# Kernel tuning notes

Hardware: AMD Instinct MI355X
Metric: run time of the kernel (lower is better)

Reference implementation:

```python
import jax, jax.numpy as jnp
import numpy as np

N_AGENTS, T, B, S = 8, 128, 64, 16
D_STATE, E, HH = 128, 64, 128


def _hyper(x, k1, b1, k2, b2):
    return jax.nn.relu(x @ k1 + b1) @ k2 + b2


def _perm_pos(n_agents, tb, s):
    # pos[row, a] = position of agent a in a random grand-coalition permutation
    keys = jax.random.split(jax.random.key(42), tb * s)
    pos = jax.vmap(lambda k: jax.random.permutation(k, n_agents))(keys)
    return pos.reshape(tb, s, n_agents)


def setup_inputs() -> dict:
    key = jax.random.key(0)
    ks = jax.random.split(key, 12)
    def rn(k, shape, scale=0.05):
        return jax.random.normal(k, shape, jnp.float32) * scale
    return {
        "q_vals": rn(ks[0], (N_AGENTS, T, B), 1.0),
        "states": rn(ks[1], (T * B, D_STATE), 1.0),
        "hw1_k1": rn(ks[2], (D_STATE, HH)), "hw1_b1": jnp.zeros((HH,), jnp.float32),
        "hw1_k2": rn(ks[3], (HH, 2 * E)), "hw1_b2": jnp.zeros((2 * E,), jnp.float32),
        "b1_k": rn(ks[4], (D_STATE, E)), "b1_b": jnp.zeros((E,), jnp.float32),
        "hw2_k1": rn(ks[5], (D_STATE, HH)), "hw2_b1": jnp.zeros((HH,), jnp.float32),
        "hw2_k2": rn(ks[6], (HH, E)), "hw2_b2": jnp.zeros((E,), jnp.float32),
        "hb2_k1": rn(ks[7], (D_STATE, E)), "hb2_b1": jnp.zeros((E,), jnp.float32),
        "hb2_k2": rn(ks[8], (E, 1)), "hb2_b2": jnp.zeros((1,), jnp.float32),
    }


def _forward(pos, q_vals, states, hw1_k1, hw1_b1, hw1_k2, hw1_b2, b1_k, b1_b,
             hw2_k1, hw2_b1, hw2_k2, hw2_b2, hb2_k1, hb2_b1, hb2_k2, hb2_b2):
    n, t, b = q_vals.shape
    tb = t * b
    q = jnp.transpose(q_vals, (1, 2, 0)).reshape(tb, n)          # agent_qs, (tb, n)
    qb = jnp.broadcast_to(q[:, None, :], (tb, S, n))
    inv = jnp.argsort(pos, axis=-1)                               # agent at each position
    q_ord = jnp.take_along_axis(qb, inv, axis=-1)                 # q ordered by position
    csum_excl = jnp.cumsum(q_ord, axis=-1) - q_ord                # sum over strictly-earlier positions
    coal_sum = jnp.take_along_axis(csum_excl, pos, axis=-1)       # sum of preceding agents' q
    coal_norm = coal_sum / jnp.maximum(pos, 1).astype(q.dtype)    # mean (0 if no predecessors)
    # Hypernets depend only on states -> compute once per tb row, broadcast over (S, n)
    w1 = jnp.abs(_hyper(states, hw1_k1, hw1_b1, hw1_k2, hw1_b2)).reshape(tb, 1, 1, 2, E)
    b1 = (states @ b1_k + b1_b).reshape(tb, 1, 1, E)
    w2 = jnp.abs(_hyper(states, hw2_k1, hw2_b1, hw2_k2, hw2_b2)).reshape(tb, 1, 1, E)
    b2 = _hyper(states, hb2_k1, hb2_b1, hb2_k2, hb2_b2).reshape(tb, 1, 1)
    hidden = jax.nn.elu(coal_norm[..., None] * w1[..., 0, :]
                        + qb[..., None] * w1[..., 1, :] + b1)     # (tb, S, n, E)
    y = jnp.sum(hidden * w2, axis=-1) + b2                        # (tb, S, n)
    alpha = jnp.abs(y).reshape(t, b, S, n).mean(axis=2)           # mean over samples
    return jnp.transpose(alpha, (2, 0, 1))                        # (n, t, b)


def reference(q_vals, states, hw1_k1, hw1_b1, hw1_k2, hw1_b2, b1_k, b1_b,
              hw2_k1, hw2_b1, hw2_k2, hw2_b2, hb2_k1, hb2_b1, hb2_k2, hb2_b2):
    n, t, b = q_vals.shape
    pos = _perm_pos(n, t * b, S)
    return _forward(pos, q_vals, states, hw1_k1, hw1_b1, hw1_k2, hw1_b2, b1_k, b1_b,
                    hw2_k1, hw2_b1, hw2_k2, hw2_b2, hb2_k1, hb2_b1, hb2_k2, hb2_b2)
```

## Files before the change

kernel.cpp:

```cpp
#include <hip/hip_runtime.h>
#include <stdint.h>

#define N_AG   8
#define S_SAMP 16
#define TB     8192
#define DST    128
#define E_DIM  64

#define RPB    8
#define CN_STR 9

#define WT1K1  0
#define WT2K1  16384
#define WT1K2  32768
#define WTM3   49152
#define WT2K2  65536
#define WT_ELEMS 73728

typedef __attribute__((ext_vector_type(8))) short  short8v;
typedef __attribute__((ext_vector_type(4))) float  float4v;

__device__ __forceinline__ float4 ld4(const float* p) { return *(const float4*)p; }

__device__ __forceinline__ unsigned short f2bf(float f) {
  uint32_t x = __float_as_uint(f);
  return (unsigned short)((x + 0x7FFFu + ((x >> 16) & 1u)) >> 16);
}
__device__ __forceinline__ uint32_t pk2(float lo, float hi) {
  return (uint32_t)f2bf(lo) | ((uint32_t)f2bf(hi) << 16);
}

__device__ __forceinline__ uint2 tf2x32(uint32_t k0, uint32_t k1,
                                        uint32_t c0, uint32_t c1) {
  uint32_t ks2 = k0 ^ k1 ^ 0x1BD11BDAu;
  uint32_t x0 = c0 + k0, x1 = c1 + k1;
#define TFR(r) { x0 += x1; x1 = (x1 << (r)) | (x1 >> (32 - (r))); x1 ^= x0; }
  TFR(13) TFR(15) TFR(26) TFR(6)
  x0 += k1;  x1 += ks2 + 1u;
  TFR(17) TFR(29) TFR(16) TFR(24)
  x0 += ks2; x1 += k0 + 2u;
  TFR(13) TFR(15) TFR(26) TFR(6)
  x0 += k0;  x1 += k1 + 3u;
  TFR(17) TFR(29) TFR(16) TFR(24)
  x0 += k1;  x1 += ks2 + 4u;
  TFR(13) TFR(15) TFR(26) TFR(6)
  x0 += ks2; x1 += k0 + 5u;
#undef TFR
  return make_uint2(x0, x1);
}

__device__ __forceinline__ short8v rdfrag(const unsigned short* base, int row, int ks, int lhi) {
  const int b = (row * 256 + ks * 64 + lhi * 16) ^ ((row & 7) << 4);
  return *(const short8v*)((const char*)base + b);
}
__device__ __forceinline__ void wrbf(unsigned short* pan, int r, int c, float v) {
  const int b = (r * 256 + c * 2) ^ ((r & 7) << 4);
  *(unsigned short*)((char*)pan + b) = f2bf(v);
}
__device__ __forceinline__ short8v gfrag(const unsigned short* wt, int n, int ks, int lhi) {
  return *(const short8v*)(wt + (n << 7) + ks * 32 + lhi * 8);
}

__global__ __launch_bounds__(256)
void wt_transpose(const float* __restrict__ hw1_k1, const float* __restrict__ hw2_k1,
                  const float* __restrict__ hw1_k2, const float* __restrict__ b1_k,
                  const float* __restrict__ hb2_k1, const float* __restrict__ hw2_k2,
                  unsigned short* __restrict__ wt)
{
  __shared__ float t[32][33];
  const int b = blockIdx.x;
  const float* src; int ldn, t0, dstbase;
  if (b < 16)      { src = hw1_k1; ldn = 128; t0 = b;      dstbase = WT1K1; }
  else if (b < 32) { src = hw2_k1; ldn = 128; t0 = b - 16; dstbase = WT2K1; }
  else if (b < 48) { src = hw1_k2; ldn = 128; t0 = b - 32; dstbase = WT1K2; }
  else if (b < 56) { src = b1_k;   ldn = 64;  t0 = b - 48; dstbase = WTM3; }
  else if (b < 64) { src = hb2_k1; ldn = 64;  t0 = b - 56; dstbase = WTM3 + 64 * 128; }
  else             { src = hw2_k2; ldn = 64;  t0 = b - 64; dstbase = WT2K2; }
  const int kt = t0 & 3, nt = t0 >> 2;
  const int tid = threadIdx.x;
  {
    const int c = tid & 31;
    for (int r = tid >> 5; r < 32; r += 8)
      t[r][c] = src[(size_t)(kt * 32 + r) * ldn + nt * 32 + c];
  }
  __syncthreads();
  {
    const int c2 = tid & 15;
    for (int n = tid >> 4; n < 32; n += 16) {
      const uint32_t v = pk2(t[2 * c2][n], t[2 * c2 + 1][n]);
      *(uint32_t*)&wt[dstbase + (nt * 32 + n) * 128 + kt * 32 + 2 * c2] = v;
    }
  }
}

__global__ __launch_bounds__(256, 4)
void alpha_mfma2(const float* __restrict__ q_vals,
                 const float* __restrict__ states,
                 const float* __restrict__ hw1_b1, const float* __restrict__ hw1_b2,
                 const float* __restrict__ b1_b,   const float* __restrict__ hw2_b1,
                 const float* __restrict__ hw2_b2, const float* __restrict__ hb2_b1,
                 const float* __restrict__ hb2_k2, const float* __restrict__ hb2_b2,
                 const unsigned short* __restrict__ wt,
                 float* __restrict__ out)
{
  __shared__ unsigned short xbf[RPB * 128];
  __shared__ unsigned short h1bf[RPB * 128];
  __shared__ unsigned short h2bf[RPB * 128];
  __shared__ float w1l[RPB][132];
  __shared__ float b1l[RPB][68];
  __shared__ float w2l[RPB][68];
  __shared__ float hbl[RPB][68];
  __shared__ float b2l[RPB];
  __shared__ float ql[RPB][N_AG];
  __shared__ float cn_l[RPB][S_SAMP][CN_STR];

  const int tid  = threadIdx.x;
  const int row0 = blockIdx.x * RPB;
  const int lane = tid & 63;
  const int wv   = tid >> 6;
  const int lrow = lane & 15;
  const int lhi  = lane >> 4;

  {
    const int r = tid >> 5, k0 = (tid & 31) * 4;
    const float4 v = ld4(&states[(size_t)(row0 + r) * DST + k0]);
    const int b = (r * 256 + k0 * 2) ^ ((r & 7) << 4);
    *(uint32_t*)((char*)xbf + b)     = pk2(v.x, v.y);
    *(uint32_t*)((char*)xbf + b + 4) = pk2(v.z, v.w);
  }
  if (tid < RPB * N_AG) {
    const int rr = tid >> 3, a = tid & 7;
    ql[rr][a] = q_vals[a * TB + row0 + rr];
  }
  __syncthreads();

  if (tid < RPB * S_SAMP) {
    const int r  = tid >> 4;
    const int sl = tid & 15;
    const uint32_t j = (uint32_t)(row0 + r) * (uint32_t)S_SAMP + (uint32_t)sl;
    uint2 kj  = tf2x32(0u, 42u, 0u, j);
    uint2 sub = tf2x32(kj.x, kj.y, 0u, 1u);
    uint32_t K[N_AG];
#pragma unroll
    for (int i = 0; i < N_AG; ++i) {
      uint2 b = tf2x32(sub.x, sub.y, 0u, (uint32_t)i);
      K[i] = b.x ^ b.y;
    }
    int posa[N_AG];
#pragma unroll
    for (int i = 0; i < N_AG; ++i) {
      int rank = 0;
#pragma unroll
      for (int m = 0; m < N_AG; ++m)
        rank += (K[m] < K[i]) || (K[m] == K[i] && m < i);
      posa[rank] = i;
    }
#pragma unroll
    for (int a = 0; a < N_AG; ++a) {
      const int pa = posa[a];
      float cs = 0.f;
#pragma unroll
      for (int a2 = 0; a2 < N_AG; ++a2)
        cs += (posa[a2] < pa) ? ql[r][a2] : 0.f;
      cn_l[r][sl][a] = cs / (float)max(pa, 1);
    }
  }

  {
    float4v a0 = {0.f,0.f,0.f,0.f}, a1 = {0.f,0.f,0.f,0.f};
    const int c0 = wv * 32 + lrow, c1 = c0 + 16;
#pragma unroll
    for (int ks = 0; ks < 4; ++ks) {
      const short8v af  = rdfrag(xbf, lrow & 7, ks, lhi);
      const short8v b0  = gfrag(wt + WT1K1, c0, ks, lhi);
      const short8v b1f = gfrag(wt + WT1K1, c1, ks, lhi);
      a0 = __builtin_amdgcn_mfma_f32_16x16x32_bf16(af, b0,  a0, 0, 0, 0);
      a1 = __builtin_amdgcn_mfma_f32_16x16x32_bf16(af, b1f, a1, 0, 0, 0);
    }
    if (lhi < 2) {
      const float bv0 = hw1_b1[c0], bv1 = hw1_b1[c1];
#pragma unroll
      for (int j = 0; j < 4; ++j) {
        const int r = lhi * 4 + j;
        wrbf(h1bf, r, c0, fmaxf(a0[j] + bv0, 0.f));
        wrbf(h1bf, r, c1, fmaxf(a1[j] + bv1, 0.f));
      }
    }
  }

  {
    float4v a0 = {0.f,0.f,0.f,0.f}, a1 = {0.f,0.f,0.f,0.f};
    const int c0 = wv * 32 + lrow, c1 = c0 + 16;
#pragma unroll
    for (int ks = 0; ks < 4; ++ks) {
      const short8v af  = rdfrag(xbf, lrow & 7, ks, lhi);
      const short8v b0  = gfrag(wt + WT2K1, c0, ks, lhi);
      const short8v b1f = gfrag(wt + WT2K1, c1, ks, lhi);
      a0 = __builtin_amdgcn_mfma_f32_16x16x32_bf16(af, b0,  a0, 0, 0, 0);
      a1 = __builtin_amdgcn_mfma_f32_16x16x32_bf16(af, b1f, a1, 0, 0, 0);
    }
    if (lhi < 2) {
      const float bv0 = hw2_b1[c0], bv1 = hw2_b1[c1];
#pragma unroll
      for (int j = 0; j < 4; ++j) {
        const int r = lhi * 4 + j;
        wrbf(h2bf, r, c0, fmaxf(a0[j] + bv0, 0.f));
        wrbf(h2bf, r, c1, fmaxf(a1[j] + bv1, 0.f));
      }
    }
  }

  {
    float4v a0 = {0.f,0.f,0.f,0.f}, a1 = {0.f,0.f,0.f,0.f};
    const int c0 = wv * 32 + lrow, c1 = c0 + 16;
#pragma unroll
    for (int ks = 0; ks < 4; ++ks) {
      const short8v af  = rdfrag(xbf, lrow & 7, ks, lhi);
      const short8v b0  = gfrag(wt + WTM3, c0, ks, lhi);
      const short8v b1f = gfrag(wt + WTM3, c1, ks, lhi);
      a0 = __builtin_amdgcn_mfma_f32_16x16x32_bf16(af, b0,  a0, 0, 0, 0);
      a1 = __builtin_amdgcn_mfma_f32_16x16x32_bf16(af, b1f, a1, 0, 0, 0);
    }
    if (lhi < 2) {
#pragma unroll
      for (int j = 0; j < 4; ++j) {
        const int r = lhi * 4 + j;
        if (c0 < 64) b1l[r][c0] = a0[j] + b1_b[c0];
        else         hbl[r][c0 - 64] = fmaxf(a0[j] + hb2_b1[c0 - 64], 0.f);
        if (c1 < 64) b1l[r][c1] = a1[j] + b1_b[c1];
        else         hbl[r][c1 - 64] = fmaxf(a1[j] + hb2_b1[c1 - 64], 0.f);
      }
    }
  }
  __syncthreads();

  if (tid < RPB * S_SAMP) {
    const int r = tid >> 4, sl = tid & 15;
    float v = hbl[r][sl]      * hb2_k2[sl]
            + hbl[r][sl + 16] * hb2_k2[sl + 16]
            + hbl[r][sl + 32] * hb2_k2[sl + 32]
            + hbl[r][sl + 48] * hb2_k2[sl + 48];
    v += __shfl_down(v, 8, 16); v += __shfl_down(v, 4, 16);
    v += __shfl_down(v, 2, 16); v += __shfl_down(v, 1, 16);
    if (sl == 0) b2l[r] = v + hb2_b2[0];
  }

  {
    float4v a0 = {0.f,0.f,0.f,0.f}, a1 = {0.f,0.f,0.f,0.f};
    const int c0 = wv * 32 + lrow, c1 = c0 + 16;
#pragma unroll
    for (int ks = 0; ks < 4; ++ks) {
      const short8v af  = rdfrag(h1bf, lrow & 7, ks, lhi);
      const short8v b0  = gfrag(wt + WT1K2, c0, ks, lhi);
      const short8v b1f = gfrag(wt + WT1K2, c1, ks, lhi);
      a0 = __builtin_amdgcn_mfma_f32_16x16x32_bf16(af, b0,  a0, 0, 0, 0);
      a1 = __builtin_amdgcn_mfma_f32_16x16x32_bf16(af, b1f, a1, 0, 0, 0);
    }
    if (lhi < 2) {
      const float bv0 = hw1_b2[c0], bv1 = hw1_b2[c1];
#pragma unroll
      for (int j = 0; j < 4; ++j) {
        const int r = lhi * 4 + j;
        w1l[r][c0] = fabsf(a0[j] + bv0);
        w1l[r][c1] = fabsf(a1[j] + bv1);
      }
    }
  }

  {
    float4v a0 = {0.f,0.f,0.f,0.f};
    const int c = wv * 16 + lrow;
#pragma unroll
    for (int ks = 0; ks < 4; ++ks) {
      const short8v af = rdfrag(h2bf, lrow & 7, ks, lhi);
      const short8v b0 = gfrag(wt + WT2K2, c, ks, lhi);
      a0 = __builtin_amdgcn_mfma_f32_16x16x32_bf16(af, b0, a0, 0, 0, 0);
    }
    if (lhi < 2) {
      const float bv = hw2_b2[c];
#pragma unroll
      for (int j = 0; j < 4; ++j)
        w2l[lhi * 4 + j][c] = fabsf(a0[j] + bv);
    }
  }
  __syncthreads();

  {
    const int sl = tid & 15;
    const int r  = (tid >> 4) & 7;
    const int a0i = (tid >> 7) * 4;
    float cn[4], qv[4], y[4];
#pragma unroll
    for (int jj = 0; jj < 4; ++jj) {
      cn[jj] = cn_l[r][sl][a0i + jj];
      qv[jj] = ql[r][a0i + jj];
      y[jj]  = 0.f;
    }
#pragma unroll 4
    for (int e = 0; e < E_DIM; e += 4) {
      const float4 wa  = ld4(&w1l[r][e]);
      const float4 wb  = ld4(&w1l[r][64 + e]);
      const float4 bb  = ld4(&b1l[r][e]);
      const float4 w2v = ld4(&w2l[r][e]);
#pragma unroll
      for (int jj = 0; jj < 4; ++jj) {
        float h;
        h = fmaf(cn[jj], wa.x, fmaf(qv[jj], wb.x, bb.x));
        y[jj] = fmaf((h > 0.f) ? h : (__expf(h) - 1.f), w2v.x, y[jj]);
        h = fmaf(cn[jj], wa.y, fmaf(qv[jj], wb.y, bb.y));
        y[jj] = fmaf((h > 0.f) ? h : (__expf(h) - 1.f), w2v.y, y[jj]);
        h = fmaf(cn[jj], wa.z, fmaf(qv[jj], wb.z, bb.z));
        y[jj] = fmaf((h > 0.f) ? h : (__expf(h) - 1.f), w2v.z, y[jj]);
        h = fmaf(cn[jj], wa.w, fmaf(qv[jj], wb.w, bb.w));
        y[jj] = fmaf((h > 0.f) ? h : (__expf(h) - 1.f), w2v.w, y[jj]);
      }
    }
    const float b2v = b2l[r];
#pragma unroll
    for (int jj = 0; jj < 4; ++jj)
      cn_l[r][sl][a0i + jj] = fabsf(y[jj] + b2v);
  }
  __syncthreads();

  if (tid < RPB * N_AG) {
    const int rr = tid & 7, a = tid >> 3;
    float acc = 0.f;
#pragma unroll
    for (int ss = 0; ss < S_SAMP; ++ss) acc += cn_l[rr][ss][a];
    out[a * TB + row0 + rr] = acc * (1.0f / (float)S_SAMP);
  }
}

#define FB_RPB 16
#define FB_H_PAD 132
#define FB_E_PAD 68
__global__ __launch_bounds__(256)
void alpha_fused2(const float* __restrict__ q_vals, const float* __restrict__ states,
                  const float* __restrict__ hw1_k1, const float* __restrict__ hw1_b1,
                  const float* __restrict__ hw1_k2, const float* __restrict__ hw1_b2,
                  const float* __restrict__ b1_k,   const float* __restrict__ b1_b,
                  const float* __restrict__ hw2_k1, const float* __restrict__ hw2_b1,
                  const float* __restrict__ hw2_k2, const float* __restrict__ hw2_b2,
                  const float* __restrict__ hb2_k1, const float* __restrict__ hb2_b1,
                  const float* __restrict__ hb2_k2, const float* __restrict__ hb2_b2,
                  float* __restrict__ out)
{
  __shared__ float s_lds[FB_RPB][DST];
  __shared__ float scratch[FB_RPB][FB_H_PAD];
  __shared__ float scratch2[FB_RPB][FB_E_PAD];
  __shared__ float w1l[FB_RPB][FB_H_PAD];
  __shared__ float b1l[FB_RPB][FB_E_PAD];
  __shared__ float w2l[FB_RPB][FB_E_PAD];
  __shared__ float b2l[FB_RPB];
  __shared__ float qlf[FB_RPB][N_AG];
  __shared__ float cnred[FB_RPB][S_SAMP][N_AG];
  const int tid = threadIdx.x;
  const int row0 = blockIdx.x * FB_RPB;
  const int r = tid >> 4, sl = tid & 15;
  {
    const float4* src = reinterpret_cast<const float4*>(states + (size_t)row0 * DST);
    reinterpret_cast<float4*>(&s_lds[0][0])[tid]       = src[tid];
    reinterpret_cast<float4*>(&s_lds[0][0])[tid + 256] = src[tid + 256];
  }
  if (tid < FB_RPB * N_AG) {
    const int rr = tid >> 3, a = tid & 7;
    qlf[rr][a] = q_vals[a * TB + row0 + rr];
  }
  __syncthreads();
  {
    const uint32_t j = (uint32_t)(row0 + r) * (uint32_t)S_SAMP + (uint32_t)sl;
    uint2 kj = tf2x32(0u, 42u, 0u, j);
    uint2 sub = tf2x32(kj.x, kj.y, 0u, 1u);
    uint32_t K[N_AG];
#pragma unroll
    for (int i = 0; i < N_AG; ++i) { uint2 b = tf2x32(sub.x, sub.y, 0u, (uint32_t)i); K[i] = b.x ^ b.y; }
    int posa[N_AG];
#pragma unroll
    for (int i = 0; i < N_AG; ++i) {
      int rank = 0;
#pragma unroll
      for (int m = 0; m < N_AG; ++m) rank += (K[m] < K[i]) || (K[m] == K[i] && m < i);
      posa[rank] = i;
    }
#pragma unroll
    for (int a = 0; a < N_AG; ++a) {
      const int pa = posa[a];
      float cs = 0.f;
#pragma unroll
      for (int a2 = 0; a2 < N_AG; ++a2) cs += (posa[a2] < pa) ? qlf[r][a2] : 0.f;
      cnred[r][sl][a] = cs / (float)max(pa, 1);
    }
  }
  {
    int c = tid & 127, rg = tid >> 7;
    float a0=0.f,a1=0.f,a2=0.f,a3=0.f,a4=0.f,a5=0.f,a6=0.f,a7=0.f;
#pragma unroll 2
    for (int k = 0; k < DST; ++k) {
      float wv = hw1_k1[k * 128 + c];
      a0 += s_lds[rg*8+0][k]*wv; a1 += s_lds[rg*8+1][k]*wv;
      a2 += s_lds[rg*8+2][k]*wv; a3 += s_lds[rg*8+3][k]*wv;
      a4 += s_lds[rg*8+4][k]*wv; a5 += s_lds[rg*8+5][k]*wv;
      a6 += s_lds[rg*8+6][k]*wv; a7 += s_lds[rg*8+7][k]*wv;
    }
    float b = hw1_b1[c];
    scratch[rg*8+0][c]=fmaxf(a0+b,0.f); scratch[rg*8+1][c]=fmaxf(a1+b,0.f);
    scratch[rg*8+2][c]=fmaxf(a2+b,0.f); scratch[rg*8+3][c]=fmaxf(a3+b,0.f);
    scratch[rg*8+4][c]=fmaxf(a4+b,0.f); scratch[rg*8+5][c]=fmaxf(a5+b,0.f);
    scratch[rg*8+6][c]=fmaxf(a6+b,0.f); scratch[rg*8+7][c]=fmaxf(a7+b,0.f);
  }
  {
    int c = tid & 63, rg = tid >> 6;
    float a0=0.f,a1=0.f,a2=0.f,a3=0.f;
#pragma unroll 2
    for (int k = 0; k < DST; ++k) {
      float wv = b1_k[k * 64 + c];
      a0 += s_lds[rg*4+0][k]*wv; a1 += s_lds[rg*4+1][k]*wv;
      a2 += s_lds[rg*4+2][k]*wv; a3 += s_lds[rg*4+3][k]*wv;
    }
    float b = b1_b[c];
    b1l[rg*4+0][c]=a0+b; b1l[rg*4+1][c]=a1+b; b1l[rg*4+2][c]=a2+b; b1l[rg*4+3][c]=a3+b;
  }
  __syncthreads();
  {
    int c = tid & 127, rg = tid >> 7;
    float a0=0.f,a1=0.f,a2=0.f,a3=0.f,a4=0.f,a5=0.f,a6=0.f,a7=0.f;
#pragma unroll 2
    for (int k = 0; k < DST; ++k) {
      float wv = hw1_k2[k * 128 + c];
      a0 += scratch[rg*8+0][k]*wv; a1 += scratch[rg*8+1][k]*wv;
      a2 += scratch[rg*8+2][k]*wv; a3 += scratch[rg*8+3][k]*wv;
      a4 += scratch[rg*8+4][k]*wv; a5 += scratch[rg*8+5][k]*wv;
      a6 += scratch[rg*8+6][k]*wv; a7 += scratch[rg*8+7][k]*wv;
    }
    float b = hw1_b2[c];
    w1l[rg*8+0][c]=fabsf(a0+b); w1l[rg*8+1][c]=fabsf(a1+b);
    w1l[rg*8+2][c]=fabsf(a2+b); w1l[rg*8+3][c]=fabsf(a3+b);
    w1l[rg*8+4][c]=fabsf(a4+b); w1l[rg*8+5][c]=fabsf(a5+b);
    w1l[rg*8+6][c]=fabsf(a6+b); w1l[rg*8+7][c]=fabsf(a7+b);
  }
  {
    int c = tid & 63, rg = tid >> 6;
    float a0=0.f,a1=0.f,a2=0.f,a3=0.f;
#pragma unroll 2
    for (int k = 0; k < DST; ++k) {
      float wv = hb2_k1[k * 64 + c];
      a0 += s_lds[rg*4+0][k]*wv; a1 += s_lds[rg*4+1][k]*wv;
      a2 += s_lds[rg*4+2][k]*wv; a3 += s_lds[rg*4+3][k]*wv;
    }
    float b = hb2_b1[c];
    scratch2[rg*4+0][c]=fmaxf(a0+b,0.f); scratch2[rg*4+1][c]=fmaxf(a1+b,0.f);
    scratch2[rg*4+2][c]=fmaxf(a2+b,0.f); scratch2[rg*4+3][c]=fmaxf(a3+b,0.f);
  }
  __syncthreads();
  {
    int c = tid & 127, rg = tid >> 7;
    float a0=0.f,a1=0.f,a2=0.f,a3=0.f,a4=0.f,a5=0.f,a6=0.f,a7=0.f;
#pragma unroll 2
    for (int k = 0; k < DST; ++k) {
      float wv = hw2_k1[k * 128 + c];
      a0 += s_lds[rg*8+0][k]*wv; a1 += s_lds[rg*8+1][k]*wv;
      a2 += s_lds[rg*8+2][k]*wv; a3 += s_lds[rg*8+3][k]*wv;
      a4 += s_lds[rg*8+4][k]*wv; a5 += s_lds[rg*8+5][k]*wv;
      a6 += s_lds[rg*8+6][k]*wv; a7 += s_lds[rg*8+7][k]*wv;
    }
    float b = hw2_b1[c];
    scratch[rg*8+0][c]=fmaxf(a0+b,0.f); scratch[rg*8+1][c]=fmaxf(a1+b,0.f);
    scratch[rg*8+2][c]=fmaxf(a2+b,0.f); scratch[rg*8+3][c]=fmaxf(a3+b,0.f);
    scratch[rg*8+4][c]=fmaxf(a4+b,0.f); scratch[rg*8+5][c]=fmaxf(a5+b,0.f);
    scratch[rg*8+6][c]=fmaxf(a6+b,0.f); scratch[rg*8+7][c]=fmaxf(a7+b,0.f);
  }
  if (tid < FB_RPB * S_SAMP) {
    float v = scratch2[r][sl]      * hb2_k2[sl]
            + scratch2[r][sl + 16] * hb2_k2[sl + 16]
            + scratch2[r][sl + 32] * hb2_k2[sl + 32]
            + scratch2[r][sl + 48] * hb2_k2[sl + 48];
    v += __shfl_down(v, 8, 16); v += __shfl_down(v, 4, 16);
    v += __shfl_down(v, 2, 16); v += __shfl_down(v, 1, 16);
    if (sl == 0) b2l[r] = v + hb2_b2[0];
  }
  __syncthreads();
  {
    int c = tid & 63, rg = tid >> 6;
    float a0=0.f,a1=0.f,a2=0.f,a3=0.f;
#pragma unroll 2
    for (int k = 0; k < DST; ++k) {
      float wv = hw2_k2[k * 64 + c];
      a0 += scratch[rg*4+0][k]*wv; a1 += scratch[rg*4+1][k]*wv;
      a2 += scratch[rg*4+2][k]*wv; a3 += scratch[rg*4+3][k]*wv;
    }
    float b = hw2_b2[c];
    w2l[rg*4+0][c]=fabsf(a0+b); w2l[rg*4+1][c]=fabsf(a1+b);
    w2l[rg*4+2][c]=fabsf(a2+b); w2l[rg*4+3][c]=fabsf(a3+b);
  }
  __syncthreads();
  {
    float cn[N_AG], qv[N_AG], y[N_AG];
#pragma unroll
    for (int a = 0; a < N_AG; ++a) { cn[a]=cnred[r][sl][a]; qv[a]=qlf[r][a]; y[a]=0.f; }
#pragma unroll 4
    for (int e = 0; e < E_DIM; e += 4) {
      const float4 wa  = ld4(&w1l[r][e]);
      const float4 wb  = ld4(&w1l[r][64 + e]);
      const float4 bb  = ld4(&b1l[r][e]);
      const float4 w2v = ld4(&w2l[r][e]);
#pragma unroll
      for (int a = 0; a < N_AG; ++a) {
        float h;
        h = fmaf(cn[a], wa.x, fmaf(qv[a], wb.x, bb.x));
        y[a] = fmaf((h > 0.f) ? h : (__expf(h) - 1.f), w2v.x, y[a]);
        h = fmaf(cn[a], wa.y, fmaf(qv[a], wb.y, bb.y));
        y[a] = fmaf((h > 0.f) ? h : (__expf(h) - 1.f), w2v.y, y[a]);
        h = fmaf(cn[a], wa.z, fmaf(qv[a], wb.z, bb.z));
        y[a] = fmaf((h > 0.f) ? h : (__expf(h) - 1.f), w2v.z, y[a]);
        h = fmaf(cn[a], wa.w, fmaf(qv[a], wb.w, bb.w));
        y[a] = fmaf((h > 0.f) ? h : (__expf(h) - 1.f), w2v.w, y[a]);
      }
    }
    const float b2v = b2l[r];
#pragma unroll
    for (int a = 0; a < N_AG; ++a) cnred[r][sl][a] = fabsf(y[a] + b2v);
  }
  __syncthreads();
  if (tid < FB_RPB * N_AG) {
    const int a = tid >> 4, rr = tid & 15;
    float acc = 0.f;
#pragma unroll
    for (int ss = 0; ss < S_SAMP; ++ss) acc += cnred[rr][ss][a];
    out[a * TB + row0 + rr] = acc * (1.0f / (float)S_SAMP);
  }
}

extern "C" void kernel_launch(void* const* d_in, const int* in_sizes, int n_in,
                              void* d_out, int out_size, void* d_ws, size_t ws_size,
                              hipStream_t stream) {
  const float* q_vals = (const float*)d_in[0];
  const float* states = (const float*)d_in[1];
  const float* hw1_k1 = (const float*)d_in[2];
  const float* hw1_b1 = (const float*)d_in[3];
  const float* hw1_k2 = (const float*)d_in[4];
  const float* hw1_b2 = (const float*)d_in[5];
  const float* b1_k   = (const float*)d_in[6];
  const float* b1_b   = (const float*)d_in[7];
  const float* hw2_k1 = (const float*)d_in[8];
  const float* hw2_b1 = (const float*)d_in[9];
  const float* hw2_k2 = (const float*)d_in[10];
  const float* hw2_b2 = (const float*)d_in[11];
  const float* hb2_k1 = (const float*)d_in[12];
  const float* hb2_b1 = (const float*)d_in[13];
  const float* hb2_k2 = (const float*)d_in[14];
  const float* hb2_b2 = (const float*)d_in[15];
  float* out = (float*)d_out;

  const size_t need = (size_t)WT_ELEMS * sizeof(unsigned short);
  if (ws_size >= need) {
    unsigned short* wt = (unsigned short*)d_ws;
    wt_transpose<<<dim3(72), 256, 0, stream>>>(
        hw1_k1, hw2_k1, hw1_k2, b1_k, hb2_k1, hw2_k2, wt);
    alpha_mfma2<<<dim3(TB / RPB), 256, 0, stream>>>(
        q_vals, states, hw1_b1, hw1_b2, b1_b, hw2_b1, hw2_b2, hb2_b1,
        hb2_k2, hb2_b2, wt, out);
  } else {
    alpha_fused2<<<dim3(TB / FB_RPB), 256, 0, stream>>>(
        q_vals, states, hw1_k1, hw1_b1, hw1_k2, hw1_b2, b1_k, b1_b,
        hw2_k1, hw2_b1, hw2_k2, hw2_b2, hb2_k1, hb2_b1, hb2_k2, hb2_b2, out);
  }
}
```

Baseline: 41.64 us.

## Process 16 rows per block with 512 threads to fill MFMA row tiles

Doubles rows per block from 8 to 16 and threads from 256 to 512, so each 16x16 MFMA tile uses all 16 A-rows instead of wasting half on duplicated rows. Each wave now computes a single 16-column output tile per GEMM, and the later elementwise and reduction stages are remapped to the new row and thread counts. Per-row weight fragment loads from global memory are amortised over twice as many rows. The cost is a larger shared-memory footprint and fewer, bigger blocks (512 blocks), which may reduce occupancy. The parts of the kernel not shown (state staging, permutation code) must also handle 16 rows, which cannot be confirmed here.

```diff
diff --git a/kernel.cpp b/kernel.cpp
--- a/kernel.cpp
+++ b/kernel.cpp
@@ -7,7 +7,7 @@
 #define DST    128
 #define E_DIM  64
 
-#define RPB    8
+#define RPB    16
 #define CN_STR 9
 
 #define WT1K1  0
@@ -93,8 +93,8 @@
   }
 }
 
-__global__ __launch_bounds__(256, 4)
-void alpha_mfma2(const float* __restrict__ q_vals,
+__global__ __launch_bounds__(512, 4)
+void alpha_mfma3(const float* __restrict__ q_vals,
                  const float* __restrict__ states,
                  const float* __restrict__ hw1_b1, const float* __restrict__ hw1_b2,
                  const float* __restrict__ b1_b,   const float* __restrict__ hw2_b1,
@@ -167,69 +167,51 @@
   }
 
   {
-    float4v a0 = {0.f,0.f,0.f,0.f}, a1 = {0.f,0.f,0.f,0.f};
-    const int c0 = wv * 32 + lrow, c1 = c0 + 16;
+    float4v a0 = {0.f,0.f,0.f,0.f};
+    const int c = wv * 16 + lrow;
 #pragma unroll
     for (int ks = 0; ks < 4; ++ks) {
-      const short8v af  = rdfrag(xbf, lrow & 7, ks, lhi);
-      const short8v b0  = gfrag(wt + WT1K1, c0, ks, lhi);
-      const short8v b1f = gfrag(wt + WT1K1, c1, ks, lhi);
-      a0 = __builtin_amdgcn_mfma_f32_16x16x32_bf16(af, b0,  a0, 0, 0, 0);
-      a1 = __builtin_amdgcn_mfma_f32_16x16x32_bf16(af, b1f, a1, 0, 0, 0);
-    }
-    if (lhi < 2) {
-      const float bv0 = hw1_b1[c0], bv1 = hw1_b1[c1];
-#pragma unroll
-      for (int j = 0; j < 4; ++j) {
-        const int r = lhi * 4 + j;
-        wrbf(h1bf, r, c0, fmaxf(a0[j] + bv0, 0.f));
-        wrbf(h1bf, r, c1, fmaxf(a1[j] + bv1, 0.f));
-      }
-    }
-  }
-
-  {
-    float4v a0 = {0.f,0.f,0.f,0.f}, a1 = {0.f,0.f,0.f,0.f};
-    const int c0 = wv * 32 + lrow, c1 = c0 + 16;
+      const short8v af = rdfrag(xbf, lrow, ks, lhi);
+      a0 = __builtin_amdgcn_mfma_f32_16x16x32_bf16(af, gfrag(wt + WT1K1, c, ks, lhi), a0, 0, 0, 0);
+    }
+    const float bv = hw1_b1[c];
+#pragma unroll
+    for (int j = 0; j < 4; ++j)
+      wrbf(h1bf, lhi * 4 + j, c, fmaxf(a0[j] + bv, 0.f));
+  }
+
+  {
+    float4v a0 = {0.f,0.f,0.f,0.f};
+    const int c = wv * 16 + lrow;
 #pragma unroll
     for (int ks = 0; ks < 4; ++ks) {
-      const short8v af  = rdfrag(xbf, lrow & 7, ks, lhi);
-      const short8v b0  = gfrag(wt + WT2K1, c0, ks, lhi);
-      const short8v b1f = gfrag(wt + WT2K1, c1, ks, lhi);
-      a0 = __builtin_amdgcn_mfma_f32_16x16x32_bf16(af, b0,  a0, 0, 0, 0);
-      a1 = __builtin_amdgcn_mfma_f32_16x16x32_bf16(af, b1f, a1, 0, 0, 0);
-    }
-    if (lhi < 2) {
-      const float bv0 = hw2_b1[c0], bv1 = hw2_b1[c1];
-#pragma unroll
-      for (int j = 0; j < 4; ++j) {
-        const int r = lhi * 4 + j;
-        wrbf(h2bf, r, c0, fmaxf(a0[j] + bv0, 0.f));
-        wrbf(h2bf, r, c1, fmaxf(a1[j] + bv1, 0.f));
-      }
-    }
-  }
-
-  {
-    float4v a0 = {0.f,0.f,0.f,0.f}, a1 = {0.f,0.f,0.f,0.f};
-    const int c0 = wv * 32 + lrow, c1 = c0 + 16;
+      const short8v af = rdfrag(xbf, lrow, ks, lhi);
+      a0 = __builtin_amdgcn_mfma_f32_16x16x32_bf16(af, gfrag(wt + WT2K1, c, ks, lhi), a0, 0, 0, 0);
+    }
+    const float bv = hw2_b1[c];
+#pragma unroll
+    for (int j = 0; j < 4; ++j)
+      wrbf(h2bf, lhi * 4 + j, c, fmaxf(a0[j] + bv, 0.f));
+  }
+
+  {
+    float4v a0 = {0.f,0.f,0.f,0.f};
+    const int c = wv * 16 + lrow;
 #pragma unroll
     for (int ks = 0; ks < 4; ++ks) {
-      const short8v af  = rdfrag(xbf, lrow & 7, ks, lhi);
-      const short8v b0  = gfrag(wt + WTM3, c0, ks, lhi);
-      const short8v b1f = gfrag(wt + WTM3, c1, ks, lhi);
-      a0 = __builtin_amdgcn_mfma_f32_16x16x32_bf16(af, b0,  a0, 0, 0, 0);
-      a1 = __builtin_amdgcn_mfma_f32_16x16x32_bf16(af, b1f, a1, 0, 0, 0);
-    }
-    if (lhi < 2) {
-#pragma unroll
-      for (int j = 0; j < 4; ++j) {
-        const int r = lhi * 4 + j;
-        if (c0 < 64) b1l[r][c0] = a0[j] + b1_b[c0];
-        else         hbl[r][c0 - 64] = fmaxf(a0[j] + hb2_b1[c0 - 64], 0.f);
-        if (c1 < 64) b1l[r][c1] = a1[j] + b1_b[c1];
-        else         hbl[r][c1 - 64] = fmaxf(a1[j] + hb2_b1[c1 - 64], 0.f);
-      }
+      const short8v af = rdfrag(xbf, lrow, ks, lhi);
+      a0 = __builtin_amdgcn_mfma_f32_16x16x32_bf16(af, gfrag(wt + WTM3, c, ks, lhi), a0, 0, 0, 0);
+    }
+    if (c < 64) {
+      const float bv = b1_b[c];
+#pragma unroll
+      for (int j = 0; j < 4; ++j)
+        b1l[lhi * 4 + j][c] = a0[j] + bv;
+    } else {
+      const float bv = hb2_b1[c - 64];
+#pragma unroll
+      for (int j = 0; j < 4; ++j)
+        hbl[lhi * 4 + j][c - 64] = fmaxf(a0[j] + bv, 0.f);
     }
   }
   __syncthreads();
@@ -246,49 +228,38 @@
   }
 
   {
-    float4v a0 = {0.f,0.f,0.f,0.f}, a1 = {0.f,0.f,0.f,0.f};
-    const int c0 = wv * 32 + lrow, c1 = c0 + 16;
-#pragma unroll
-    for (int ks = 0; ks < 4; ++ks) {
-      const short8v af  = rdfrag(h1bf, lrow & 7, ks, lhi);
-      const short8v b0  = gfrag(wt + WT1K2, c0, ks, lhi);
-      const short8v b1f = gfrag(wt + WT1K2, c1, ks, lhi);
-      a0 = __builtin_amdgcn_mfma_f32_16x16x32_bf16(af, b0,  a0, 0, 0, 0);
-      a1 = __builtin_amdgcn_mfma_f32_16x16x32_bf16(af, b1f, a1, 0, 0, 0);
-    }
-    if (lhi < 2) {
-      const float bv0 = hw1_b2[c0], bv1 = hw1_b2[c1];
-#pragma unroll
-      for (int j = 0; j < 4; ++j) {
-        const int r = lhi * 4 + j;
-        w1l[r][c0] = fabsf(a0[j] + bv0);
-        w1l[r][c1] = fabsf(a1[j] + bv1);
-      }
-    }
-  }
-
-  {
     float4v a0 = {0.f,0.f,0.f,0.f};
     const int c = wv * 16 + lrow;
 #pragma unroll
     for (int ks = 0; ks < 4; ++ks) {
-      const short8v af = rdfrag(h2bf, lrow & 7, ks, lhi);
-      const short8v b0 = gfrag(wt + WT2K2, c, ks, lhi);
-      a0 = __builtin_amdgcn_mfma_f32_16x16x32_bf16(af, b0, a0, 0, 0, 0);
-    }
-    if (lhi < 2) {
-      const float bv = hw2_b2[c];
-#pragma unroll
-      for (int j = 0; j < 4; ++j)
-        w2l[lhi * 4 + j][c] = fabsf(a0[j] + bv);
-    }
-  }
-  __syncthreads();
-
-  {
-    const int sl = tid & 15;
-    const int r  = (tid >> 4) & 7;
-    const int a0i = (tid >> 7) * 4;
+      const short8v af = rdfrag(h1bf, lrow, ks, lhi);
+      a0 = __builtin_amdgcn_mfma_f32_16x16x32_bf16(af, gfrag(wt + WT1K2, c, ks, lhi), a0, 0, 0, 0);
+    }
+    const float bv = hw1_b2[c];
+#pragma unroll
+    for (int j = 0; j < 4; ++j)
+      w1l[lhi * 4 + j][c] = fabsf(a0[j] + bv);
+  }
+
+  if (wv < 4) {
+    float4v a0 = {0.f,0.f,0.f,0.f};
+    const int c = wv * 16 + lrow;
+#pragma unroll
+    for (int ks = 0; ks < 4; ++ks) {
+      const short8v af = rdfrag(h2bf, lrow, ks, lhi);
+      a0 = __builtin_amdgcn_mfma_f32_16x16x32_bf16(af, gfrag(wt + WT2K2, c, ks, lhi), a0, 0, 0, 0);
+    }
+    const float bv = hw2_b2[c];
+#pragma unroll
+    for (int j = 0; j < 4; ++j)
+      w2l[lhi * 4 + j][c] = fabsf(a0[j] + bv);
+  }
+  __syncthreads();
+
+  {
+    const int sl  = tid & 15;
+    const int r   = (tid >> 4) & 15;
+    const int a0i = (tid >> 8) * 4;
     float cn[4], qv[4], y[4];
 #pragma unroll
     for (int jj = 0; jj < 4; ++jj) {
@@ -323,7 +294,7 @@
   __syncthreads();
 
   if (tid < RPB * N_AG) {
-    const int rr = tid & 7, a = tid >> 3;
+    const int rr = tid & 15, a = tid >> 4;
     float acc = 0.f;
 #pragma unroll
     for (int ss = 0; ss < S_SAMP; ++ss) acc += cn_l[rr][ss][a];
@@ -556,7 +527,7 @@
     unsigned short* wt = (unsigned short*)d_ws;
     wt_transpose<<<dim3(72), 256, 0, stream>>>(
         hw1_k1, hw2_k1, hw1_k2, b1_k, hb2_k1, hw2_k2, wt);
-    alpha_mfma2<<<dim3(TB / RPB), 256, 0, stream>>>(
+    alpha_mfma3<<<dim3(TB / RPB), 512, 0, stream>>>(
         q_vals, states, hw1_b1, hw1_b2, b1_b, hw2_b1, hw2_b2, hb2_b1,
         hb2_k2, hb2_b2, wt, out);
   } else {
```

New measurement: 33.99 us. -18.4%, faster.
